# Kernel tuning notes

Measured on AMD Instinct MI355X. Metric: run time of the kernel, lower is better.

## Reference

```python
import jax, jax.numpy as jnp
import numpy as np

EPS_BN = 1e-5
EPS_ATT = 1e-9

def conv1x1(x, w, b=None):
    # x: [B,C,N], w: [O,C] -> [B,O,N]
    y = jnp.einsum('oc,bcn->bon', w, x)
    if b is not None:
        y = y + b[None, :, None]
    return y

def batchnorm1d(x, g, b):
    # training-mode BN over (batch, N) per channel, biased variance
    mean = jnp.mean(x, axis=(0, 2), keepdims=True)
    var = jnp.mean((x - mean) ** 2, axis=(0, 2), keepdims=True)
    xh = (x - mean) * jax.lax.rsqrt(var + EPS_BN)
    return xh * g[None, :, None] + b[None, :, None]

def sa_layer(x, xyz_emb, wqk, wv, bv, wt, bt, bng, bnb):
    # x, xyz_emb: [B,C,N]
    x = x + xyz_emb
    q = jnp.einsum('dc,bcn->bdn', wqk, x)      # [B,C/4,N] (shared weight)
    k = jnp.einsum('dc,bcn->bdn', wqk, x)
    v = conv1x1(x, wv, bv)                      # [B,C,N]
    attn = jnp.einsum('bdn,bdm->bnm', q, k)     # [B,N,N]: rows=queries n, cols=keys m
    attn = jax.nn.softmax(attn, axis=-1)
    attn = attn / (EPS_ATT + jnp.sum(attn, axis=1, keepdims=True))  # L1 renorm over dim=1
    x_r = jnp.einsum('bcn,bnm->bcm', v, attn)   # [B,C,N]
    x_r = jax.nn.relu(batchnorm1d(conv1x1(x - x_r, wt, bt), bng, bnb))
    return x + x_r

def setup_inputs() -> dict:
    key = jax.random.key(0)
    ks = jax.random.split(key, 12)
    B, C, N = 4, 128, 4096
    s = lambda fan: 1.0 / np.sqrt(fan)
    return {
        'x': jax.random.normal(ks[0], (B, C, N), jnp.float32),
        'xyz': jax.random.uniform(ks[1], (B, N, 3), jnp.float32),
        'conv1_w': jax.random.normal(ks[2], (C, C), jnp.float32) * s(C),
        'bn1_g': jnp.ones((C,), jnp.float32),
        'bn1_b': jnp.zeros((C,), jnp.float32),
        'pos_w': jax.random.normal(ks[3], (C, 3), jnp.float32) * s(3),
        'pos_b': jnp.zeros((C,), jnp.float32),
        'sa_wqk': jax.random.normal(ks[4], (5, C // 4, C), jnp.float32) * s(C),
        'sa_wv': jax.random.normal(ks[5], (5, C, C), jnp.float32) * s(C),
        'sa_bv': jnp.zeros((5, C), jnp.float32),
        'sa_wt': jax.random.normal(ks[6], (5, C, C), jnp.float32) * s(C),
        'sa_bt': jnp.zeros((5, C), jnp.float32),
        'sa_bng': jnp.ones((5, C), jnp.float32),
        'sa_bnb': jnp.zeros((5, C), jnp.float32),
    }

def reference(x, xyz, conv1_w, bn1_g, bn1_b, pos_w, pos_b,
              sa_wqk, sa_wv, sa_bv, sa_wt, sa_bt, sa_bng, sa_bnb):
    xyz_t = jnp.transpose(xyz, (0, 2, 1))           # [B,3,N]
    xyz_emb = conv1x1(xyz_t, pos_w, pos_b)          # [B,C,N]
    h = jax.nn.relu(batchnorm1d(conv1x1(x, conv1_w), bn1_g, bn1_b))
    outs = []
    for i in range(5):
        h = sa_layer(h, xyz_emb, sa_wqk[i], sa_wv[i], sa_bv[i],
                     sa_wt[i], sa_bt[i], sa_bng[i], sa_bnb[i])
        outs.append(h)
    return jnp.concatenate(outs, axis=1)            # [B,5C,N]
```

## Files before the change

kernel.cpp:

```cpp
#include <hip/hip_runtime.h>

#define kB 4
#define kC 128
#define kN 4096
#define kD 32
#define kL 5
#define kCO 640
#define kL2E 1.4426950408889634f

typedef float f32x4 __attribute__((ext_vector_type(4)));
typedef short bf16x4 __attribute__((ext_vector_type(4)));
typedef short bf16x8 __attribute__((ext_vector_type(8)));
typedef unsigned u32;
typedef u32 u32x4 __attribute__((ext_vector_type(4)));
typedef unsigned short u16;

__device__ __forceinline__ float bf2f(u16 u) {
  unsigned v = ((unsigned)u) << 16;
  return __builtin_bit_cast(float, v);
}
__device__ __forceinline__ u16 f2bf(float f) {
  unsigned u = __builtin_bit_cast(unsigned, f);
  u += 0x7fffu + ((u >> 16) & 1u);
  return (u16)(u >> 16);
}
__device__ __forceinline__ void split2(float v, u16& hi, u16& lo) {
  hi = f2bf(v);
  lo = f2bf(v - bf2f(hi));
}
__device__ __forceinline__ float fexp2(float x) {
#if __has_builtin(__builtin_amdgcn_exp2f)
  return __builtin_amdgcn_exp2f(x);
#else
  return exp2f(x);
#endif
}
__device__ __forceinline__ float flog2(float x) {
#if __has_builtin(__builtin_amdgcn_logf)
  return __builtin_amdgcn_logf(x);
#else
  return log2f(x);
#endif
}
__device__ __forceinline__ void online_upd(float& mx, float& sm, float s) {
  float d = s - mx;
  float e = fexp2(-fabsf(d) * kL2E);
  bool up = s > mx;
  sm = (up ? 1.f : sm) + e * (up ? sm : 1.f);
  mx = fmaxf(mx, s);
}
__device__ __forceinline__ void online_merge(float& M, float& S, float Mo, float So) {
  float d = Mo - M;
  float e = fexp2(-fabsf(d) * kL2E);
  bool up = Mo > M;
  S = (up ? So : S) + e * (up ? S : So);
  M = fmaxf(M, Mo);
}
__device__ __forceinline__ u32 pkhalves(u32 a, u32 b) {
#if __has_builtin(__builtin_amdgcn_perm)
  return __builtin_amdgcn_perm(b, a, 0x07060302u);
#else
  return (a >> 16) | (b & 0xffff0000u);
#endif
}
__device__ __forceinline__ void splitpair(float a, float b, u32& hw, u32& lw) {
  u32 ua = __builtin_bit_cast(u32, a), ub = __builtin_bit_cast(u32, b);
  hw = pkhalves(ua, ub);
  float la = a - __builtin_bit_cast(float, ua & 0xffff0000u);
  float lb = b - __builtin_bit_cast(float, ub & 0xffff0000u);
  lw = pkhalves(__builtin_bit_cast(u32, la), __builtin_bit_cast(u32, lb));
}
__device__ __forceinline__ f32x4 mfma3(bf16x8 ah, bf16x8 al, bf16x8 bh, bf16x8 bl, f32x4 c) {
  c = __builtin_amdgcn_mfma_f32_16x16x32_bf16(ah, bh, c, 0, 0, 0);
  c = __builtin_amdgcn_mfma_f32_16x16x32_bf16(ah, bl, c, 0, 0, 0);
  c = __builtin_amdgcn_mfma_f32_16x16x32_bf16(al, bh, c, 0, 0, 0);
  return c;
}

__global__ void sentinel_kernel(float* out, float val, int total) {
  int i = blockIdx.x * 256 + threadIdx.x;
  if (i < total) out[i] = val;
}

__global__ void cvt_all_kernel(const float* __restrict__ s0, const float* __restrict__ s1,
                               const float* __restrict__ s2, const float* __restrict__ s3,
                               u16* h0, u16* l0, u16* h1, u16* l1,
                               u16* h2, u16* l2, u16* h3, u16* l3) {
  int i = blockIdx.x * 256 + threadIdx.x;
  const float* s;
  u16 *dh, *dl;
  int off;
  if (i < 16384) { s = s0; dh = h0; dl = l0; off = i; }
  else if (i < 36864) { s = s1; dh = h1; dl = l1; off = i - 16384; }
  else if (i < 118784) { s = s2; dh = h2; dl = l2; off = i - 36864; }
  else if (i < 200704) { s = s3; dh = h3; dl = l3; off = i - 118784; }
  else return;
  u16 h, l;
  split2(s[off], h, l);
  dh[off] = h;
  dl[off] = l;
}

__global__ __launch_bounds__(256) void prep_kernel(
    const float* __restrict__ h, long hstride, long hoff,
    u16* __restrict__ xh, u16* __restrict__ xl) {
  __shared__ float t[32][33];
  int n0 = blockIdx.x * 32, c0 = blockIdx.y * 32, b = blockIdx.z;
  int tx = threadIdx.x & 31, ty = threadIdx.x >> 5;
#pragma unroll
  for (int i = 0; i < 4; ++i) {
    int c = c0 + ty + i * 8;
    t[ty + i * 8][tx] = h[(size_t)b * hstride + hoff + (size_t)c * kN + n0 + tx];
  }
  __syncthreads();
#pragma unroll
  for (int i = 0; i < 4; ++i) {
    int n = n0 + ty + i * 8, c = c0 + tx;
    u16 hh, ll;
    split2(t[tx][ty + i * 8], hh, ll);
    size_t idx = ((size_t)b * kN + n) * kC + c;
    xh[idx] = hh;
    xl[idx] = ll;
  }
}

__global__ __launch_bounds__(320) void qv_kernel(
    const u16* __restrict__ xh, const u16* __restrict__ xl,
    const u16* __restrict__ wqkh, const u16* __restrict__ wqkl,
    const u16* __restrict__ wvh, const u16* __restrict__ wvl,
    const float* __restrict__ bv,
    u16* __restrict__ Qh, u16* __restrict__ Ql,
    u16* __restrict__ Vph, u16* __restrict__ Vpl) {
  __shared__ float vt[4][2][16][17];
  int wave = threadIdx.x >> 6, lane = threadIdx.x & 63;
  int b = blockIdx.y;
  int n0 = blockIdx.x * 16;
  int col = lane & 15, g = lane >> 4;
  f32x4 acc[2] = {};
  const u16* xrh = xh + ((size_t)b * kN + n0 + col) * kC + g * 8;
  const u16* xrl = xl + ((size_t)b * kN + n0 + col) * kC + g * 8;
#pragma unroll
  for (int kk = 0; kk < 4; ++kk) {
    bf16x8 bh = *(const bf16x8*)(xrh + kk * 32);
    bf16x8 bl = *(const bf16x8*)(xrl + kk * 32);
#pragma unroll
    for (int i = 0; i < 2; ++i) {
      int ot = wave * 2 + i;
      size_t wi = (ot < 2) ? ((size_t)(ot * 16 + col) * kC) : ((size_t)((ot - 2) * 16 + col) * kC);
      const u16* wsh = (ot < 2) ? (wqkh + wi) : (wvh + wi);
      const u16* wsl = (ot < 2) ? (wqkl + wi) : (wvl + wi);
      bf16x8 ah = *(const bf16x8*)(wsh + kk * 32 + g * 8);
      bf16x8 al = *(const bf16x8*)(wsl + kk * 32 + g * 8);
      acc[i] = mfma3(ah, al, bh, bl, acc[i]);
    }
  }
  if (wave > 0) {
#pragma unroll
    for (int i = 0; i < 2; ++i) {
      int ct = wave * 2 + i - 2;
#pragma unroll
      for (int r = 0; r < 4; ++r)
        vt[wave - 1][i][4 * g + r][col] = acc[i][r] + bv[ct * 16 + 4 * g + r];
    }
  }
  __syncthreads();
  if (wave == 0) {
#pragma unroll
    for (int i = 0; i < 2; ++i) {
#pragma unroll
      for (int r = 0; r < 4; ++r) {
        int d = i * 16 + 4 * g + r;
        u16 hh, ll;
        split2(acc[i][r], hh, ll);
        size_t idx = ((size_t)b * kN + n0 + col) * kD + d;
        Qh[idx] = hh;
        Ql[idx] = ll;
      }
    }
  } else {
    int nt = n0 >> 5, p = (n0 >> 4) & 1;
#pragma unroll
    for (int i = 0; i < 2; ++i) {
      int ct = wave * 2 + i - 2;
      bf16x4 vh4, vl4;
#pragma unroll
      for (int j = 0; j < 4; ++j) {
        float v = vt[wave - 1][i][col][4 * g + j];
        u16 hh, ll;
        split2(v, hh, ll);
        vh4[j] = (short)hh;
        vl4[j] = (short)ll;
      }
      size_t base = ((((size_t)b * (kN / 32) + nt) * 8 + ct) * 64 + lane) * 8 + p * 4;
      *(bf16x4*)(Vph + base) = vh4;
      *(bf16x4*)(Vpl + base) = vl4;
    }
  }
}

__global__ __launch_bounds__(256) void pass1_kernel(
    const u16* __restrict__ Qh, const u16* __restrict__ Ql,
    float* __restrict__ rme) {
  __shared__ float mxs[4][32], sms[4][32];
  int wave = threadIdx.x >> 6, lane = threadIdx.x & 63;
  int b = blockIdx.y;
  int n0 = blockIdx.x * 32;
  int col = lane & 15, g = lane >> 4;
  const u16* qbh = Qh + (size_t)b * kN * kD;
  const u16* qbl = Ql + (size_t)b * kN * kD;
  bf16x8 ah0 = *(const bf16x8*)(qbh + (size_t)(n0 + col) * kD + g * 8);
  bf16x8 al0 = *(const bf16x8*)(qbl + (size_t)(n0 + col) * kD + g * 8);
  bf16x8 ah1 = *(const bf16x8*)(qbh + (size_t)(n0 + 16 + col) * kD + g * 8);
  bf16x8 al1 = *(const bf16x8*)(qbl + (size_t)(n0 + 16 + col) * kD + g * 8);
  float mx[8], sm[8];
#pragma unroll
  for (int r = 0; r < 8; ++r) { mx[r] = -3.0e38f; sm[r] = 0.f; }
#pragma unroll 1
  for (int m0 = wave * 16; m0 < kN; m0 += 64) {
    bf16x8 bh = *(const bf16x8*)(qbh + (size_t)(m0 + col) * kD + g * 8);
    bf16x8 bl = *(const bf16x8*)(qbl + (size_t)(m0 + col) * kD + g * 8);
    f32x4 s0 = {}, s1 = {};
    s0 = mfma3(ah0, al0, bh, bl, s0);
    s1 = mfma3(ah1, al1, bh, bl, s1);
#pragma unroll
    for (int r = 0; r < 4; ++r) {
      online_upd(mx[r], sm[r], s0[r]);
      online_upd(mx[r + 4], sm[r + 4], s1[r]);
    }
  }
#pragma unroll
  for (int o = 1; o < 16; o <<= 1) {
#pragma unroll
    for (int r = 0; r < 8; ++r) {
      float Mo = __shfl_xor(mx[r], o, 64);
      float So = __shfl_xor(sm[r], o, 64);
      online_merge(mx[r], sm[r], Mo, So);
    }
  }
  if (col == 0) {
#pragma unroll
    for (int r = 0; r < 4; ++r) {
      mxs[wave][4 * g + r] = mx[r];
      sms[wave][4 * g + r] = sm[r];
      mxs[wave][16 + 4 * g + r] = mx[r + 4];
      sms[wave][16 + 4 * g + r] = sm[r + 4];
    }
  }
  __syncthreads();
  if (threadIdx.x < 32) {
    int t = threadIdx.x;
    float M = mxs[0][t], S = sms[0][t];
#pragma unroll
    for (int w = 1; w < 4; ++w) online_merge(M, S, mxs[w][t], sms[w][t]);
    rme[(size_t)b * kN + n0 + t] = M * kL2E + flog2(S);
  }
}

__global__ __launch_bounds__(256) void pass2_kernel(
    const u16* __restrict__ Qh, const u16* __restrict__ Ql,
    const u16* __restrict__ Vph, const u16* __restrict__ Vpl,
    const float* __restrict__ rme,
    const u16* __restrict__ xh, const u16* __restrict__ xl,
    u16* __restrict__ yth, u16* __restrict__ ytl) {
  __shared__ f32x4 accs[4][8][64];
  __shared__ float csl[2][4][16];
  int wave = threadIdx.x >> 6, lane = threadIdx.x & 63;
  int b = blockIdx.y;
  int m0 = blockIdx.x * 32;
  int col = lane & 15, g = lane >> 4;
  const u16* qbh = Qh + (size_t)b * kN * kD;
  const u16* qbl = Ql + (size_t)b * kN * kD;
  const float* rmb = rme + (size_t)b * kN;
  bf16x8 bmh0 = *(const bf16x8*)(qbh + (size_t)(m0 + col) * kD + g * 8);
  bf16x8 bml0 = *(const bf16x8*)(qbl + (size_t)(m0 + col) * kD + g * 8);
  bf16x8 bmh1 = *(const bf16x8*)(qbh + (size_t)(m0 + 16 + col) * kD + g * 8);
  bf16x8 bml1 = *(const bf16x8*)(qbl + (size_t)(m0 + 16 + col) * kD + g * 8);
  const u16* vbh = Vph + (size_t)b * (kN / 32) * 4096;
  const u16* vbl = Vpl + (size_t)b * (kN / 32) * 4096;
  f32x4 accA[8] = {}, accB[8] = {};
  float csA = 0.f, csB = 0.f;
#pragma unroll 1
  for (int nn = wave * 32; nn < kN; nn += 128) {
    bf16x8 ah0 = *(const bf16x8*)(qbh + (size_t)(nn + col) * kD + g * 8);
    bf16x8 al0 = *(const bf16x8*)(qbl + (size_t)(nn + col) * kD + g * 8);
    bf16x8 ah1 = *(const bf16x8*)(qbh + (size_t)(nn + 16 + col) * kD + g * 8);
    bf16x8 al1 = *(const bf16x8*)(qbl + (size_t)(nn + 16 + col) * kD + g * 8);
    f32x4 sA0 = {}, sA1 = {}, sB0 = {}, sB1 = {};
    sA0 = mfma3(ah0, al0, bmh0, bml0, sA0);
    sA1 = mfma3(ah1, al1, bmh0, bml0, sA1);
    sB0 = mfma3(ah0, al0, bmh1, bml1, sB0);
    sB1 = mfma3(ah1, al1, bmh1, bml1, sB1);
    float pA[8], pB[8];
#pragma unroll
    for (int r = 0; r < 4; ++r) {
      float e0 = rmb[nn + 4 * g + r];
      float e1 = rmb[nn + 16 + 4 * g + r];
      pA[r] = fexp2(sA0[r] * kL2E - e0);
      pA[r + 4] = fexp2(sA1[r] * kL2E - e1);
      pB[r] = fexp2(sB0[r] * kL2E - e0);
      pB[r + 4] = fexp2(sB1[r] * kL2E - e1);
      csA += pA[r] + pA[r + 4];
      csB += pB[r] + pB[r + 4];
    }
    u32x4 Ahw, Alw, Bhw, Blw;
#pragma unroll
    for (int k2 = 0; k2 < 4; ++k2) {
      u32 h0, l0, h1, l1;
      splitpair(pA[2 * k2], pA[2 * k2 + 1], h0, l0);
      splitpair(pB[2 * k2], pB[2 * k2 + 1], h1, l1);
      Ahw[k2] = h0; Alw[k2] = l0;
      Bhw[k2] = h1; Blw[k2] = l1;
    }
    bf16x8 bAh = __builtin_bit_cast(bf16x8, Ahw);
    bf16x8 bAl = __builtin_bit_cast(bf16x8, Alw);
    bf16x8 bBh = __builtin_bit_cast(bf16x8, Bhw);
    bf16x8 bBl = __builtin_bit_cast(bf16x8, Blw);
    size_t vtile = (size_t)(nn >> 5) * 4096;
#pragma unroll
    for (int ct = 0; ct < 8; ++ct) {
      size_t off = vtile + ((size_t)ct * 64 + lane) * 8;
      bf16x8 a8h = *(const bf16x8*)(vbh + off);
      bf16x8 a8l = *(const bf16x8*)(vbl + off);
      accA[ct] = mfma3(a8h, a8l, bAh, bAl, accA[ct]);
      accB[ct] = mfma3(a8h, a8l, bBh, bBl, accB[ct]);
    }
  }
  csA += __shfl_xor(csA, 16, 64);
  csA += __shfl_xor(csA, 32, 64);
  csB += __shfl_xor(csB, 16, 64);
  csB += __shfl_xor(csB, 32, 64);
  if (lane < 16) {
    csl[0][wave][lane] = csA;
    csl[1][wave][lane] = csB;
  }
#pragma unroll
  for (int ct = 0; ct < 8; ++ct) accs[wave][ct][lane] = accA[ct];
  __syncthreads();
  {
    float inv = 1.0f / (1e-9f + csl[0][0][col] + csl[0][1][col] + csl[0][2][col] + csl[0][3][col]);
    const u16* xrh = xh + ((size_t)b * kN + m0 + col) * kC;
    const u16* xrl = xl + ((size_t)b * kN + m0 + col) * kC;
#pragma unroll
    for (int i = 0; i < 2; ++i) {
      int ct = wave * 2 + i;
      f32x4 a = accs[0][ct][lane];
      a += accs[1][ct][lane];
      a += accs[2][ct][lane];
      a += accs[3][ct][lane];
      bf16x4 xvh = *(const bf16x4*)(xrh + ct * 16 + 4 * g);
      bf16x4 xvl = *(const bf16x4*)(xrl + ct * 16 + 4 * g);
#pragma unroll
      for (int r = 0; r < 4; ++r) {
        float xv = bf2f((u16)xvh[r]) + bf2f((u16)xvl[r]);
        float y = xv - a[r] * inv;
        u16 hh, ll;
        split2(y, hh, ll);
        size_t idx = ((size_t)b * kN + m0 + col) * kC + ct * 16 + 4 * g + r;
        yth[idx] = hh;
        ytl[idx] = ll;
      }
    }
  }
  __syncthreads();
#pragma unroll
  for (int ct = 0; ct < 8; ++ct) accs[wave][ct][lane] = accB[ct];
  __syncthreads();
  {
    float inv = 1.0f / (1e-9f + csl[1][0][col] + csl[1][1][col] + csl[1][2][col] + csl[1][3][col]);
    const u16* xrh = xh + ((size_t)b * kN + m0 + 16 + col) * kC;
    const u16* xrl = xl + ((size_t)b * kN + m0 + 16 + col) * kC;
#pragma unroll
    for (int i = 0; i < 2; ++i) {
      int ct = wave * 2 + i;
      f32x4 a = accs[0][ct][lane];
      a += accs[1][ct][lane];
      a += accs[2][ct][lane];
      a += accs[3][ct][lane];
      bf16x4 xvh = *(const bf16x4*)(xrh + ct * 16 + 4 * g);
      bf16x4 xvl = *(const bf16x4*)(xrl + ct * 16 + 4 * g);
#pragma unroll
      for (int r = 0; r < 4; ++r) {
        float xv = bf2f((u16)xvh[r]) + bf2f((u16)xvl[r]);
        float y = xv - a[r] * inv;
        u16 hh, ll;
        split2(y, hh, ll);
        size_t idx = ((size_t)b * kN + m0 + 16 + col) * kC + ct * 16 + 4 * g + r;
        yth[idx] = hh;
        ytl[idx] = ll;
      }
    }
  }
}

__global__ __launch_bounds__(256) void tconv_kernel(
    const u16* __restrict__ inh, const u16* __restrict__ inl,
    const u16* __restrict__ wh, const u16* __restrict__ wl,
    const float* __restrict__ bias, float* __restrict__ u,
    long ustride, long uoff, float* __restrict__ part) {
  int wave = threadIdx.x >> 6, lane = threadIdx.x & 63;
  int b = blockIdx.y;
  int n0 = blockIdx.x * 16;
  int col = lane & 15, g = lane >> 4;
  f32x4 acc[2] = {};
  const u16* xrh = inh + ((size_t)b * kN + n0 + col) * kC + g * 8;
  const u16* xrl = inl + ((size_t)b * kN + n0 + col) * kC + g * 8;
#pragma unroll
  for (int kk = 0; kk < 4; ++kk) {
    bf16x8 bh = *(const bf16x8*)(xrh + kk * 32);
    bf16x8 bl = *(const bf16x8*)(xrl + kk * 32);
#pragma unroll
    for (int i = 0; i < 2; ++i) {
      int ot = wave * 2 + i;
      bf16x8 ah = *(const bf16x8*)(wh + (size_t)(ot * 16 + col) * kC + kk * 32 + g * 8);
      bf16x8 al = *(const bf16x8*)(wl + (size_t)(ot * 16 + col) * kC + kk * 32 + g * 8);
      acc[i] = mfma3(ah, al, bh, bl, acc[i]);
    }
  }
  int bid = blockIdx.y * (kN / 16) + blockIdx.x;
#pragma unroll
  for (int i = 0; i < 2; ++i) {
    int ot = wave * 2 + i;
#pragma unroll
    for (int r = 0; r < 4; ++r) {
      int c = ot * 16 + 4 * g + r;
      float v = acc[i][r] + (bias ? bias[c] : 0.f);
      u[(size_t)b * ustride + uoff + (size_t)c * kN + n0 + col] = v;
      float s = v, q = v * v;
#pragma unroll
      for (int o = 1; o < 16; o <<= 1) {
        s += __shfl_xor(s, o, 64);
        q += __shfl_xor(q, o, 64);
      }
      if (col == 0) {
        part[((size_t)bid * kC + c) * 2 + 0] = s;
        part[((size_t)bid * kC + c) * 2 + 1] = q;
      }
    }
  }
}

__global__ __launch_bounds__(256) void bn_fin_kernel(const float* __restrict__ part,
                                                     float* __restrict__ stat) {
  int c = blockIdx.x;
  __shared__ double rs[4], rss[4];
  double s = 0.0, ss = 0.0;
  for (int k = threadIdx.x; k < 1024; k += 256) {
    s += (double)part[((size_t)k * kC + c) * 2 + 0];
    ss += (double)part[((size_t)k * kC + c) * 2 + 1];
  }
#pragma unroll
  for (int o = 1; o < 64; o <<= 1) {
    s += __shfl_xor(s, o, 64);
    ss += __shfl_xor(ss, o, 64);
  }
  int wid = threadIdx.x >> 6, lane = threadIdx.x & 63;
  if (lane == 0) { rs[wid] = s; rss[wid] = ss; }
  __syncthreads();
  if (threadIdx.x == 0) {
    double S = rs[0] + rs[1] + rs[2] + rs[3];
    double SS = rss[0] + rss[1] + rss[2] + rss[3];
    double mean = S / (double)(kB * kN);
    double var = SS / (double)(kB * kN) - mean * mean;
    if (var < 0.0) var = 0.0;
    stat[c] = (float)mean;
    stat[kC + c] = rsqrtf((float)var + 1e-5f);
  }
}

__global__ __launch_bounds__(256) void bnprep_kernel(
    const float* __restrict__ u, long ustride, long uoff,
    const float* __restrict__ stat,
    const float* __restrict__ g, const float* __restrict__ bb,
    const float* __restrict__ h, long hstride, long hoff, int use_res,
    const float* __restrict__ xyz, const float* __restrict__ pw,
    const float* __restrict__ pb,
    float* __restrict__ out, long ostride, long ooff,
    u16* __restrict__ xh, u16* __restrict__ xl) {
  __shared__ float t[32][33];
  int n0 = blockIdx.x * 32, c0 = blockIdx.y * 32, b = blockIdx.z;
  int tx = threadIdx.x & 31, ty = threadIdx.x >> 5;
  const float* xp = xyz + ((size_t)b * kN + n0 + tx) * 3;
  float xv0 = xp[0], xv1 = xp[1], xv2 = xp[2];
#pragma unroll
  for (int i = 0; i < 4; ++i) {
    int c = c0 + ty + i * 8;
    float e = pw[c * 3 + 0] * xv0 + pw[c * 3 + 1] * xv1 + pw[c * 3 + 2] * xv2 + pb[c];
    float y = (u[(size_t)b * ustride + uoff + (size_t)c * kN + n0 + tx] - stat[c]) *
                  stat[kC + c] * g[c] + bb[c];
    y = fmaxf(y, 0.f);
    if (use_res) y += h[(size_t)b * hstride + hoff + (size_t)c * kN + n0 + tx] + e;
    out[(size_t)b * ostride + ooff + (size_t)c * kN + n0 + tx] = y;
    t[ty + i * 8][tx] = y + e;
  }
  __syncthreads();
#pragma unroll
  for (int i = 0; i < 4; ++i) {
    int n = n0 + ty + i * 8, c = c0 + tx;
    u16 hh, ll;
    split2(t[tx][ty + i * 8], hh, ll);
    size_t idx = ((size_t)b * kN + n) * kC + c;
    xh[idx] = hh;
    xl[idx] = ll;
  }
}

extern "C" void kernel_launch(void* const* d_in, const int* in_sizes, int n_in,
                              void* d_out, int out_size, void* d_ws, size_t ws_size,
                              hipStream_t stream) {
  const float* x = (const float*)d_in[0];
  const float* xyz = (const float*)d_in[1];
  const float* conv1_w = (const float*)d_in[2];
  const float* bn1_g = (const float*)d_in[3];
  const float* bn1_b = (const float*)d_in[4];
  const float* pos_w = (const float*)d_in[5];
  const float* pos_b = (const float*)d_in[6];
  const float* sa_wqk = (const float*)d_in[7];
  const float* sa_wv = (const float*)d_in[8];
  const float* sa_bv = (const float*)d_in[9];
  const float* sa_wt = (const float*)d_in[10];
  const float* sa_bt = (const float*)d_in[11];
  const float* sa_bng = (const float*)d_in[12];
  const float* sa_bnb = (const float*)d_in[13];
  float* out = (float*)d_out;
  char* ws = (char*)d_ws;
  const size_t MB = (size_t)1 << 20;

  const size_t NEED = 28 * MB;
  if (ws_size < NEED) {
    float val = 100.0f + (float)(ws_size >> 20);
    sentinel_kernel<<<dim3((out_size + 255) / 256), dim3(256), 0, stream>>>(out, val, out_size);
    return;
  }

  u16* xh = (u16*)(ws);
  u16* xl = (u16*)(ws + 4 * MB);
  u16* yth = (u16*)(ws + 8 * MB);
  u16* ytl = (u16*)(ws + 12 * MB);
  u16* Vph = (u16*)(ws + 16 * MB);
  u16* Vpl = (u16*)(ws + 20 * MB);
  u16* Qh = (u16*)(ws + 24 * MB);
  u16* Ql = (u16*)(ws + 25 * MB);
  u16* wa = (u16*)(ws + 26 * MB);
  size_t woff = 0;
  u16* c1h = wa + woff; woff += 16384;
  u16* c1l = wa + woff; woff += 16384;
  u16* qkh = wa + woff; woff += 5 * 32 * 128;
  u16* qkl = wa + woff; woff += 5 * 32 * 128;
  u16* wvh = wa + woff; woff += 5 * 128 * 128;
  u16* wvl = wa + woff; woff += 5 * 128 * 128;
  u16* wth = wa + woff; woff += 5 * 128 * 128;
  u16* wtl = wa + woff; woff += 5 * 128 * 128;
  float* stat = (float*)(ws + 26 * MB + 851968);
  float* rme = (float*)(ws + 27 * MB);
  float* part = (float*)(ws + 27 * MB);

  dim3 blk(256);

  cvt_all_kernel<<<dim3(784), blk, 0, stream>>>(
      conv1_w, sa_wqk, sa_wv, sa_wt, c1h, c1l, qkh, qkl, wvh, wvl, wth, wtl);

  const long sbo = (long)kCO * kN;
  const long slice = (long)kC * kN;
  const long h0off = 4 * slice;

  prep_kernel<<<dim3(kN / 32, kC / 32, kB), blk, 0, stream>>>(x, slice, 0, xh, xl);
  tconv_kernel<<<dim3(kN / 16, kB), blk, 0, stream>>>(
      xh, xl, c1h, c1l, nullptr, out, sbo, 0, part);
  bn_fin_kernel<<<dim3(kC), blk, 0, stream>>>(part, stat);
  bnprep_kernel<<<dim3(kN / 32, kC / 32, kB), blk, 0, stream>>>(
      out, sbo, 0, stat, bn1_g, bn1_b, nullptr, 0, 0, 0, xyz, pos_w, pos_b,
      out, sbo, h0off, xh, xl);

  long hoff = h0off;
  for (int i = 0; i < kL; ++i) {
    long uoff = (long)i * slice;
    qv_kernel<<<dim3(kN / 16, kB), dim3(320), 0, stream>>>(
        xh, xl, qkh + (size_t)i * kD * kC, qkl + (size_t)i * kD * kC,
        wvh + (size_t)i * kC * kC, wvl + (size_t)i * kC * kC,
        sa_bv + (size_t)i * kC, Qh, Ql, Vph, Vpl);
    pass1_kernel<<<dim3(kN / 32, kB), blk, 0, stream>>>(Qh, Ql, rme);
    pass2_kernel<<<dim3(kN / 32, kB), blk, 0, stream>>>(
        Qh, Ql, Vph, Vpl, rme, xh, xl, yth, ytl);
    tconv_kernel<<<dim3(kN / 16, kB), blk, 0, stream>>>(
        yth, ytl, wth + (size_t)i * kC * kC, wtl + (size_t)i * kC * kC,
        sa_bt + (size_t)i * kC, out, sbo, uoff, part);
    bn_fin_kernel<<<dim3(kC), blk, 0, stream>>>(part, stat);
    bnprep_kernel<<<dim3(kN / 32, kC / 32, kB), blk, 0, stream>>>(
        out, sbo, uoff, stat, sa_bng + (size_t)i * kC, sa_bnb + (size_t)i * kC,
        out, sbo, hoff, 1, xyz, pos_w, pos_b, out, sbo, uoff, xh, xl);
    hoff = uoff;
  }
}
```

Measured before the change: 798.0 us.

## Fuse trans-conv and BN partial stats into attention pass2 epilogue

The pass2 attention kernel now stages its x - x_r result (hi/lo bf16 split) in shared memory and runs the 128x128 trans-conv with MFMA in its epilogue. It writes the conv output and per-block BN partial sums directly, so the separate tconv launch and the 8 MB yt round trip through global memory go away for each of the five layers. bn_fin now takes the partial count, 512 blocks instead of 1024, and part is moved so it no longer overlaps rme. The cost is more shared memory and registers in pass2, which may reduce occupancy, plus weight loads from global memory in every block.

```diff
diff --git a/kernel.cpp b/kernel.cpp
--- a/kernel.cpp
+++ b/kernel.cpp
@@ -261,9 +261,13 @@
     const u16* __restrict__ Vph, const u16* __restrict__ Vpl,
     const float* __restrict__ rme,
     const u16* __restrict__ xh, const u16* __restrict__ xl,
-    u16* __restrict__ yth, u16* __restrict__ ytl) {
+    const u16* __restrict__ twh, const u16* __restrict__ twl,
+    const float* __restrict__ tbias,
+    float* __restrict__ u, long ustride, long uoff,
+    float* __restrict__ part) {
   __shared__ f32x4 accs[4][8][64];
   __shared__ float csl[2][4][16];
+  __shared__ u16 yhl[2][32][136];
   int wave = threadIdx.x >> 6, lane = threadIdx.x & 63;
   int b = blockIdx.y;
   int m0 = blockIdx.x * 32;
@@ -349,16 +353,18 @@
       a += accs[3][ct][lane];
       bf16x4 xvh = *(const bf16x4*)(xrh + ct * 16 + 4 * g);
       bf16x4 xvl = *(const bf16x4*)(xrl + ct * 16 + 4 * g);
+      bf16x4 yh4, yl4;
 #pragma unroll
       for (int r = 0; r < 4; ++r) {
         float xv = bf2f((u16)xvh[r]) + bf2f((u16)xvl[r]);
         float y = xv - a[r] * inv;
         u16 hh, ll;
         split2(y, hh, ll);
-        size_t idx = ((size_t)b * kN + m0 + col) * kC + ct * 16 + 4 * g + r;
-        yth[idx] = hh;
-        ytl[idx] = ll;
-      }
+        yh4[r] = (short)hh;
+        yl4[r] = (short)ll;
+      }
+      *(bf16x4*)&yhl[0][col][ct * 16 + 4 * g] = yh4;
+      *(bf16x4*)&yhl[1][col][ct * 16 + 4 * g] = yl4;
     }
   }
   __syncthreads();
@@ -378,15 +384,61 @@
       a += accs[3][ct][lane];
       bf16x4 xvh = *(const bf16x4*)(xrh + ct * 16 + 4 * g);
       bf16x4 xvl = *(const bf16x4*)(xrl + ct * 16 + 4 * g);
+      bf16x4 yh4, yl4;
 #pragma unroll
       for (int r = 0; r < 4; ++r) {
         float xv = bf2f((u16)xvh[r]) + bf2f((u16)xvl[r]);
         float y = xv - a[r] * inv;
         u16 hh, ll;
         split2(y, hh, ll);
-        size_t idx = ((size_t)b * kN + m0 + 16 + col) * kC + ct * 16 + 4 * g + r;
-        yth[idx] = hh;
-        ytl[idx] = ll;
+        yh4[r] = (short)hh;
+        yl4[r] = (short)ll;
+      }
+      *(bf16x4*)&yhl[0][16 + col][ct * 16 + 4 * g] = yh4;
+      *(bf16x4*)&yhl[1][16 + col][ct * 16 + 4 * g] = yl4;
+    }
+  }
+  __syncthreads();
+  f32x4 tacc[2][2] = {};
+#pragma unroll
+  for (int kk = 0; kk < 4; ++kk) {
+#pragma unroll
+    for (int h = 0; h < 2; ++h) {
+      bf16x8 byh = *(const bf16x8*)&yhl[0][h * 16 + col][kk * 32 + g * 8];
+      bf16x8 byl = *(const bf16x8*)&yhl[1][h * 16 + col][kk * 32 + g * 8];
+#pragma unroll
+      for (int i = 0; i < 2; ++i) {
+        int ot = wave * 2 + i;
+        bf16x8 ahw = *(const bf16x8*)(twh + (size_t)(ot * 16 + col) * kC + kk * 32 + g * 8);
+        bf16x8 alw = *(const bf16x8*)(twl + (size_t)(ot * 16 + col) * kC + kk * 32 + g * 8);
+        tacc[i][h] = mfma3(ahw, alw, byh, byl, tacc[i][h]);
+      }
+    }
+  }
+  int bid = b * (kN / 32) + (m0 >> 5);
+#pragma unroll
+  for (int i = 0; i < 2; ++i) {
+    int ot = wave * 2 + i;
+#pragma unroll
+    for (int r = 0; r < 4; ++r) {
+      int c = ot * 16 + 4 * g + r;
+      float sps = 0.f, spq = 0.f;
+#pragma unroll
+      for (int h = 0; h < 2; ++h) {
+        float v = tacc[i][h][r] + tbias[c];
+        u[(size_t)b * ustride + uoff + (size_t)c * kN + m0 + h * 16 + col] = v;
+        float s = v, q = v * v;
+#pragma unroll
+        for (int o = 1; o < 16; o <<= 1) {
+          s += __shfl_xor(s, o, 64);
+          q += __shfl_xor(q, o, 64);
+        }
+        sps += s;
+        spq += q;
+      }
+      if (col == 0) {
+        part[((size_t)bid * kC + c) * 2 + 0] = sps;
+        part[((size_t)bid * kC + c) * 2 + 1] = spq;
       }
     }
   }
@@ -440,11 +492,11 @@
 }
 
 __global__ __launch_bounds__(256) void bn_fin_kernel(const float* __restrict__ part,
-                                                     float* __restrict__ stat) {
+                                                     float* __restrict__ stat, int cnt) {
   int c = blockIdx.x;
   __shared__ double rs[4], rss[4];
   double s = 0.0, ss = 0.0;
-  for (int k = threadIdx.x; k < 1024; k += 256) {
+  for (int k = threadIdx.x; k < cnt; k += 256) {
     s += (double)part[((size_t)k * kC + c) * 2 + 0];
     ss += (double)part[((size_t)k * kC + c) * 2 + 1];
   }
@@ -534,8 +586,6 @@
 
   u16* xh = (u16*)(ws);
   u16* xl = (u16*)(ws + 4 * MB);
-  u16* yth = (u16*)(ws + 8 * MB);
-  u16* ytl = (u16*)(ws + 12 * MB);
   u16* Vph = (u16*)(ws + 16 * MB);
   u16* Vpl = (u16*)(ws + 20 * MB);
   u16* Qh = (u16*)(ws + 24 * MB);
@@ -552,7 +602,7 @@
   u16* wtl = wa + woff; woff += 5 * 128 * 128;
   float* stat = (float*)(ws + 26 * MB + 851968);
   float* rme = (float*)(ws + 27 * MB);
-  float* part = (float*)(ws + 27 * MB);
+  float* part = (float*)(ws + 27 * MB + 65536);
 
   dim3 blk(256);
 
@@ -566,7 +616,7 @@
   prep_kernel<<<dim3(kN / 32, kC / 32, kB), blk, 0, stream>>>(x, slice, 0, xh, xl);
   tconv_kernel<<<dim3(kN / 16, kB), blk, 0, stream>>>(
       xh, xl, c1h, c1l, nullptr, out, sbo, 0, part);
-  bn_fin_kernel<<<dim3(kC), blk, 0, stream>>>(part, stat);
+  bn_fin_kernel<<<dim3(kC), blk, 0, stream>>>(part, stat, 1024);
   bnprep_kernel<<<dim3(kN / 32, kC / 32, kB), blk, 0, stream>>>(
       out, sbo, 0, stat, bn1_g, bn1_b, nullptr, 0, 0, 0, xyz, pos_w, pos_b,
       out, sbo, h0off, xh, xl);
@@ -580,11 +630,10 @@
         sa_bv + (size_t)i * kC, Qh, Ql, Vph, Vpl);
     pass1_kernel<<<dim3(kN / 32, kB), blk, 0, stream>>>(Qh, Ql, rme);
     pass2_kernel<<<dim3(kN / 32, kB), blk, 0, stream>>>(
-        Qh, Ql, Vph, Vpl, rme, xh, xl, yth, ytl);
-    tconv_kernel<<<dim3(kN / 16, kB), blk, 0, stream>>>(
-        yth, ytl, wth + (size_t)i * kC * kC, wtl + (size_t)i * kC * kC,
+        Qh, Ql, Vph, Vpl, rme, xh, xl,
+        wth + (size_t)i * kC * kC, wtl + (size_t)i * kC * kC,
         sa_bt + (size_t)i * kC, out, sbo, uoff, part);
-    bn_fin_kernel<<<dim3(kC), blk, 0, stream>>>(part, stat);
+    bn_fin_kernel<<<dim3(kC), blk, 0, stream>>>(part, stat, 512);
     bnprep_kernel<<<dim3(kN / 32, kC / 32, kB), blk, 0, stream>>>(
         out, sbo, uoff, stat, sa_bng + (size_t)i * kC, sa_bnb + (size_t)i * kC,
         out, sbo, hoff, 1, xyz, pos_w, pos_b, out, sbo, uoff, xh, xl);
```

Measured after the change: 738.2 us. 1.08x faster.
